# Optimization experiments

Hardware: AMD Instinct MI355X
Metric: run time of the kernel (lower is better)

The kernel has to match this reference:

```python
import jax, jax.numpy as jnp
import numpy as np

B, T, F, C, L, W, NT, H = 4096, 64, 32, 64, 256, 512, 8, 12

# Tsit5 Butcher tableau (fixed-step, 6-stage FSAL-free form)
A21 = 0.161
A31, A32 = -0.008480655492356989, 0.335480655492357
A41, A42, A43 = 2.8971530571054935, -6.359448489975075, 4.362295432869581
A51, A52, A53, A54 = 5.325864828439257, -11.748883564062828, 7.4955393428898365, -0.09249506636175525
A61, A62, A63, A64, A65 = 5.86145544294642, -12.92096931784711, 8.159367898576159, -0.071584973281401, -0.028269050394068383
BC1, BC2, BC3, BC4, BC5, BC6 = 0.09646076681806523, 0.01, 0.4798896504144996, 1.379008574103742, -3.290069515436081, 2.324710524099774
SUBSTEPS = 10  # dt0 = 0.1, integrate each unit interval with 10 fixed steps


def setup_inputs() -> dict:
    key = jax.random.key(0)
    ks = jax.random.split(key, 16)
    def lin(k, out_d, in_d, scale=None):
        s = (1.0 / np.sqrt(in_d)) if scale is None else scale
        return jax.random.normal(k, (out_d, in_d), jnp.float32) * s
    inp = {
        "x_seq": jax.random.normal(ks[0], (B, T, F), jnp.float32),
        "country_idx": jax.random.randint(ks[1], (B,), 0, C),
        "horizon": H,
        # GRU encoder params (equinox GRUCell layout: 3*hidden stacked r,z,n)
        "W_ih": lin(ks[2], 3 * L, F + C),
        "W_hh": lin(ks[3], 3 * L, L),
        "b_ih": jnp.zeros((3 * L,), jnp.float32),
        "b_n": jnp.zeros((L,), jnp.float32),
        # NeuralField MLP 256->512->512->256, small init to keep the ODE stable
        "W0": lin(ks[4], W, L, 0.1 / np.sqrt(L)),
        "b0": jnp.zeros((W,), jnp.float32),
        "W1": lin(ks[5], W, W, 0.1 / np.sqrt(W)),
        "b1": jnp.zeros((W,), jnp.float32),
        "W2": lin(ks[6], L, W, 0.1 / np.sqrt(W)),
        "b2": jnp.zeros((L,), jnp.float32),
        # Decoder
        "W_dec": lin(ks[7], NT, L),
        "b_dec": jnp.zeros((NT,), jnp.float32),
    }
    return inp


def reference(x_seq, W_ih, W_hh, b_ih, b_n, W0, b0, W1, b1, W2, b2, W_dec, b_dec, country_idx, horizon):
    dtype = x_seq.dtype
    n_countries = W_ih.shape[1] - x_seq.shape[2]
    n_latent = W_hh.shape[1]
    ohe = jax.nn.one_hot(country_idx, n_countries, dtype=dtype)  # [B, C]

    # ---- GRU encoder scan over time ----
    h0 = jnp.zeros((x_seq.shape[0], n_latent), dtype)
    def gru_step(h, x_t):
        x_in = jnp.concatenate([x_t, ohe], axis=-1)          # [B, F+C]
        ih = x_in @ W_ih.T + b_ih                            # [B, 3L]
        hh = h @ W_hh.T                                      # [B, 3L]
        ir, iz, inn = jnp.split(ih, 3, axis=-1)
        hr, hz, hn = jnp.split(hh, 3, axis=-1)
        r = jax.nn.sigmoid(ir + hr)
        z = jax.nn.sigmoid(iz + hz)
        n = jnp.tanh(inn + r * (hn + b_n))
        return n + z * (h - n), None
    h_final, _ = jax.lax.scan(gru_step, h0, jnp.swapaxes(x_seq, 0, 1))

    # ---- Neural ODE vector field (autonomous ELU MLP) ----
    def f(y):
        a = jax.nn.elu(y @ W0.T + b0)
        a = jax.nn.elu(a @ W1.T + b1)
        return a @ W2.T + b2

    dt = jnp.asarray(1.0 / SUBSTEPS, dtype)
    def tsit5_step(y, _):
        k1 = f(y)
        k2 = f(y + dt * (A21 * k1))
        k3 = f(y + dt * (A31 * k1 + A32 * k2))
        k4 = f(y + dt * (A41 * k1 + A42 * k2 + A43 * k3))
        k5 = f(y + dt * (A51 * k1 + A52 * k2 + A53 * k3 + A54 * k4))
        k6 = f(y + dt * (A61 * k1 + A62 * k2 + A63 * k3 + A64 * k4 + A65 * k5))
        y_new = y + dt * (BC1 * k1 + BC2 * k2 + BC3 * k3 + BC4 * k4 + BC5 * k5 + BC6 * k6)
        return y_new, None

    def unit(y, _):
        y, _ = jax.lax.scan(tsit5_step, y, None, length=SUBSTEPS)
        return y, y  # save state at each integer time t = 1..horizon

    _, ys = jax.lax.scan(unit, h_final, None, length=horizon)  # [H, B, L]

    # ---- linear decode ----
    out = jnp.einsum('hbl,tl->bht', ys, W_dec) + b_dec  # [B, H, n_targets]
    return out
```

## Files before the change

### kernel.cpp

```cpp
#include <hip/hip_runtime.h>

typedef __bf16 bf16;
typedef __bf16 bf16x8 __attribute__((ext_vector_type(8)));
typedef __bf16 bf16x4 __attribute__((ext_vector_type(4)));
typedef float  f32x4  __attribute__((ext_vector_type(4)));
typedef unsigned int u32;

#define B_TOT 4096
#define T_SEQ 64
#define NT_OUT 8
#define NTHR 512
#define NBLK 256
#define GSZ  8

#define WS_W0   0
#define WS_W1   262144
#define WS_W2   786432
#define WS_WHH  1048576
#define WS_WIH  1441792
#define WS_BC   1490944
#define WS_GY   1703936
#define WS_GYB  3801088
#define WS_GH1  5898240
#define WS_GH2  10092544
#define WS_FLG  14286848
#define WS_MAP  14303232

constexpr float A21 = 0.161f;
constexpr float A31 = -0.008480655492356989f, A32 = 0.335480655492357f;
constexpr float A41 = 2.8971530571054935f, A42 = -6.359448489975075f, A43 = 4.362295432869581f;
constexpr float A51 = 5.325864828439257f, A52 = -11.748883564062828f, A53 = 7.4955393428898365f, A54 = -0.09249506636175525f;
constexpr float A61 = 5.86145544294642f, A62 = -12.92096931784711f, A63 = 8.159367898576159f, A64 = -0.071584973281401f, A65 = -0.028269050394068383f;
constexpr float BC1 = 0.09646076681806523f, BC2 = 0.01f, BC3 = 0.4798896504144996f;
constexpr float BC4 = 1.379008574103742f, BC5 = -3.290069515436081f, BC6 = 2.324710524099774f;
constexpr float DT = 0.1f;
constexpr float BROW[5][5] = {
    {A21, 0, 0, 0, 0},
    {A31, A32, 0, 0, 0},
    {A41, A42, A43, 0, 0},
    {A51, A52, A53, A54, 0},
    {A61, A62, A63, A64, A65}};
constexpr float FCF[6] = {BC1, BC2, BC3, BC4, BC5, BC6};

__device__ __forceinline__ f32x4 MFMA(bf16x8 a, bf16x8 b, f32x4 c) {
    return __builtin_amdgcn_mfma_f32_16x16x32_bf16(a, b, c, 0, 0, 0);
}
__device__ __forceinline__ float eluf(float x) { return x > 0.f ? x : __expf(x) - 1.f; }
__device__ __forceinline__ float sigm_f(float x) { return 1.f / (1.f + __expf(-x)); }
__device__ __forceinline__ float tanh_f(float x) { return 1.f - 2.f / (__expf(2.f * x) + 1.f); }

template<bool FAST>
__device__ __forceinline__ void ld4g(const bf16* p, bf16x8& a0, bf16x8& a1, bf16x8& a2, bf16x8& a3) {
    if constexpr (FAST) {
        asm volatile(
            "global_load_dwordx4 %0, %4, off sc0\n\t"
            "global_load_dwordx4 %1, %4, off offset:1024 sc0\n\t"
            "global_load_dwordx4 %2, %4, off offset:2048 sc0\n\t"
            "global_load_dwordx4 %3, %4, off offset:3072 sc0"
            : "=&v"(a0), "=&v"(a1), "=&v"(a2), "=&v"(a3) : "v"(p) : "memory");
    } else {
        asm volatile(
            "global_load_dwordx4 %0, %4, off sc0 sc1\n\t"
            "global_load_dwordx4 %1, %4, off offset:1024 sc0 sc1\n\t"
            "global_load_dwordx4 %2, %4, off offset:2048 sc0 sc1\n\t"
            "global_load_dwordx4 %3, %4, off offset:3072 sc0 sc1"
            : "=&v"(a0), "=&v"(a1), "=&v"(a2), "=&v"(a3) : "v"(p) : "memory");
    }
}
template<bool FAST>
__device__ __forceinline__ bf16x8 ld1g(const bf16* p) {
    bf16x8 a;
    if constexpr (FAST)
        asm volatile("global_load_dwordx4 %0, %1, off sc0\n\ts_waitcnt vmcnt(0)"
                     : "=v"(a) : "v"(p) : "memory");
    else
        asm volatile("global_load_dwordx4 %0, %1, off sc0 sc1\n\ts_waitcnt vmcnt(0)"
                     : "=v"(a) : "v"(p) : "memory");
    return a;
}
template<bool FAST>
__device__ __forceinline__ void st4g(bf16* p, bf16x4 v) {
    if constexpr (FAST) *(bf16x4*)p = v;
    else asm volatile("global_store_dwordx2 %0, %1, off sc0 sc1" :: "v"(p), "v"(v) : "memory");
}
template<int N>
__device__ __forceinline__ void vmwaitN() {
    asm volatile("s_waitcnt vmcnt(%0)" :: "n"(N) : "memory");
    __builtin_amdgcn_sched_barrier(0);
}

__device__ __forceinline__ void produce(u32* f, int tid) {
    asm volatile("s_waitcnt vmcnt(0)" ::: "memory");
    __syncthreads();
    if (tid == 0) __hip_atomic_fetch_add(f, 1u, __ATOMIC_RELAXED, __HIP_MEMORY_SCOPE_AGENT);
}
__device__ __forceinline__ void consume(const u32* f, u32 tgt, int tid) {
    if (tid == 0) {
        while (__hip_atomic_load(f, __ATOMIC_RELAXED, __HIP_MEMORY_SCOPE_AGENT) < tgt)
            __builtin_amdgcn_s_sleep(1);
    }
    __syncthreads();
}

template<int ST, bool FAST>
__device__ __forceinline__ void ode_stage(
    const bf16* sW0, const bf16* sW1, const bf16* sW2,
    bf16* gY, bf16* gH1, bf16* gH2,
    u32* fY, u32* fH1, u32* fH2, int tid, int w, int lane,
    const f32x4 (&b0v)[4], const f32x4 (&b1v)[4], const f32x4 (&b2v)[2],
    const int (&dA)[4], const int (&dY)[2],
    f32x4 (&yreg)[2], f32x4 (&kreg)[5][2],
    u32& eY, u32& eH1, u32& eH2) {
    const f32x4 Z = {0.f, 0.f, 0.f, 0.f};
    {
        bf16x8 a[8];
        const bf16* p = gY + w * 4096 + lane * 8;
        ld4g<FAST>(p, a[0], a[1], a[2], a[3]);
        ld4g<FAST>(p + 2048, a[4], a[5], a[6], a[7]);
        f32x4 acc[4] = {Z, Z, Z, Z};
        vmwaitN<4>();
        #pragma unroll
        for (int kk = 0; kk < 4; ++kk)
            #pragma unroll
            for (int nt = 0; nt < 4; ++nt)
                acc[nt] = MFMA(*(const bf16x8*)&sW0[(nt * 8 + kk) * 512 + lane * 8], a[kk], acc[nt]);
        vmwaitN<0>();
        #pragma unroll
        for (int kk = 4; kk < 8; ++kk)
            #pragma unroll
            for (int nt = 0; nt < 4; ++nt)
                acc[nt] = MFMA(*(const bf16x8*)&sW0[(nt * 8 + kk) * 512 + lane * 8], a[kk], acc[nt]);
        #pragma unroll
        for (int nt = 0; nt < 4; ++nt) {
            bf16x4 ov;
            #pragma unroll
            for (int r = 0; r < 4; ++r) ov[r] = (bf16)eluf(acc[nt][r] + b0v[nt][r]);
            st4g<FAST>(gH1 + w * 8192 + dA[nt], ov);
        }
    }
    produce(fH1, tid); ++eH1;
    consume(fH1, GSZ * eH1, tid);
    {
        bf16x8 a[16];
        const bf16* p = gH1 + w * 8192 + lane * 8;
        ld4g<FAST>(p, a[0], a[1], a[2], a[3]);
        ld4g<FAST>(p + 2048, a[4], a[5], a[6], a[7]);
        ld4g<FAST>(p + 4096, a[8], a[9], a[10], a[11]);
        ld4g<FAST>(p + 6144, a[12], a[13], a[14], a[15]);
        f32x4 acc[4] = {Z, Z, Z, Z};
        vmwaitN<8>();
        #pragma unroll
        for (int kk = 0; kk < 8; ++kk)
            #pragma unroll
            for (int nt = 0; nt < 4; ++nt)
                acc[nt] = MFMA(*(const bf16x8*)&sW1[(nt * 16 + kk) * 512 + lane * 8], a[kk], acc[nt]);
        vmwaitN<0>();
        #pragma unroll
        for (int kk = 8; kk < 16; ++kk)
            #pragma unroll
            for (int nt = 0; nt < 4; ++nt)
                acc[nt] = MFMA(*(const bf16x8*)&sW1[(nt * 16 + kk) * 512 + lane * 8], a[kk], acc[nt]);
        #pragma unroll
        for (int nt = 0; nt < 4; ++nt) {
            bf16x4 ov;
            #pragma unroll
            for (int r = 0; r < 4; ++r) ov[r] = (bf16)eluf(acc[nt][r] + b1v[nt][r]);
            st4g<FAST>(gH2 + w * 8192 + dA[nt], ov);
        }
    }
    produce(fH2, tid); ++eH2;
    consume(fH2, GSZ * eH2, tid);
    {
        bf16x8 a[16];
        const bf16* p = gH2 + w * 8192 + lane * 8;
        ld4g<FAST>(p, a[0], a[1], a[2], a[3]);
        ld4g<FAST>(p + 2048, a[4], a[5], a[6], a[7]);
        ld4g<FAST>(p + 4096, a[8], a[9], a[10], a[11]);
        ld4g<FAST>(p + 6144, a[12], a[13], a[14], a[15]);
        f32x4 acc[2] = {Z, Z};
        vmwaitN<8>();
        #pragma unroll
        for (int kk = 0; kk < 8; ++kk)
            #pragma unroll
            for (int nt = 0; nt < 2; ++nt)
                acc[nt] = MFMA(*(const bf16x8*)&sW2[(nt * 16 + kk) * 512 + lane * 8], a[kk], acc[nt]);
        vmwaitN<0>();
        #pragma unroll
        for (int kk = 8; kk < 16; ++kk)
            #pragma unroll
            for (int nt = 0; nt < 2; ++nt)
                acc[nt] = MFMA(*(const bf16x8*)&sW2[(nt * 16 + kk) * 512 + lane * 8], a[kk], acc[nt]);
        #pragma unroll
        for (int nt = 0; nt < 2; ++nt) {
            f32x4 kv;
            #pragma unroll
            for (int r = 0; r < 4; ++r) kv[r] = acc[nt][r] + b2v[nt][r];
            f32x4 yst;
            if constexpr (ST < 5) {
                kreg[ST][nt] = kv;
                yst = yreg[nt];
                #pragma unroll
                for (int s = 0; s <= ST; ++s) {
                    const float c = DT * BROW[ST][s];
                    #pragma unroll
                    for (int r = 0; r < 4; ++r) yst[r] += c * kreg[s][nt][r];
                }
            } else {
                #pragma unroll
                for (int s = 0; s < 5; ++s) {
                    const float c = DT * FCF[s];
                    #pragma unroll
                    for (int r = 0; r < 4; ++r) yreg[nt][r] += c * kreg[s][nt][r];
                }
                #pragma unroll
                for (int r = 0; r < 4; ++r) yreg[nt][r] += (DT * FCF[5]) * kv[r];
                yst = yreg[nt];
            }
            bf16x4 ov;
            #pragma unroll
            for (int r = 0; r < 4; ++r) ov[r] = (bf16)yst[r];
            st4g<FAST>(gY + w * 4096 + dY[nt], ov);
        }
    }
    produce(fY, tid); ++eY;
}

template<bool FAST>
__device__ __forceinline__ void dec_unit(const bf16* gY, const float* sWdec, const float* sBdec,
                                         float* out, int g, int j, int w, int lane, int H, int u) {
    const int rloc = 2 * w + (lane >> 5);
    const int li = lane & 31;
    const bf16* p = gY + (size_t)j * 4096 + (((li >> 2) * 64 + (li & 3) * 16 + rloc)) * 8;
    bf16x8 yv = ld1g<FAST>(p);
    const int f0 = li * 8;
    float acc[8];
    #pragma unroll
    for (int t = 0; t < 8; ++t) acc[t] = 0.f;
    #pragma unroll
    for (int e = 0; e < 8; ++e) {
        const float yf = (float)yv[e];
        #pragma unroll
        for (int t = 0; t < 8; ++t) acc[t] += yf * sWdec[t * 256 + f0 + e];
    }
    #pragma unroll
    for (int k = 1; k < 32; k <<= 1)
        #pragma unroll
        for (int t = 0; t < 8; ++t) acc[t] += __shfl_xor(acc[t], k, 64);
    if (li == 0) {
        const size_t row = (size_t)g * 128 + 16 * j + rloc;
        #pragma unroll
        for (int t = 0; t < 8; ++t) out[(row * H + u) * NT_OUT + t] = acc[t] + sBdec[t];
    }
}

template<bool FAST>
__device__ void body(const float* __restrict__ x_seq, const int* __restrict__ cidx,
                     const float* __restrict__ b_n, const float* __restrict__ b0,
                     const float* __restrict__ b1, const float* __restrict__ b2,
                     const float* __restrict__ W_dec, const float* __restrict__ b_dec,
                     char* __restrict__ ws, float* __restrict__ out,
                     bf16* sWgt, float* sWdec, float* sBdec,
                     int H, int g, int j) {
    const int tid = threadIdx.x, w = tid >> 6, lane = tid & 63;
    const int lm = lane & 15, q = lane >> 4, q4 = q << 2;
    const int grow0 = g * 128;

    const bf16* W0p  = (const bf16*)(ws + WS_W0);
    const bf16* W1p  = (const bf16*)(ws + WS_W1);
    const bf16* W2p  = (const bf16*)(ws + WS_W2);
    const bf16* WhhP = (const bf16*)(ws + WS_WHH);
    const bf16* WihP = (const bf16*)(ws + WS_WIH);
    const float* bias_c = (const float*)(ws + WS_BC);
    bf16* gY  = (bf16*)(ws + WS_GY)  + (size_t)g * 32768;
    bf16* gYb = (bf16*)(ws + WS_GYB) + (size_t)g * 32768;
    bf16* gH1 = (bf16*)(ws + WS_GH1) + (size_t)g * 65536;
    bf16* gH2 = (bf16*)(ws + WS_GH2) + (size_t)g * 65536;
    u32* fl  = (u32*)(ws + WS_FLG + (size_t)g * 512);
    u32 *fY = fl, *fH1 = fl + 16, *fH2 = fl + 32;

    u32 eY = 0, eH1 = 0, eH2 = 0;

    for (int i = tid; i < 2048; i += NTHR) sWdec[i] = W_dec[i];
    if (tid < 8) sBdec[tid] = b_dec[tid];
    for (int i = tid; i < 54 * 64; i += NTHR) {
        const int fr = i >> 6, l = i & 63;
        const int tau = fr / 9, kk = fr % 9;
        const int gam = tau >> 1, p = tau & 1;
        const int c = gam * 16 + 2 * j + p;
        const bf16* src = (kk < 8) ? &WhhP[(((size_t)c) * 8 + kk) * 512 + l * 8]
                                   : &WihP[((size_t)c) * 512 + l * 8];
        *(bf16x8*)&sWgt[((size_t)fr) * 512 + l * 8] = *(const bf16x8*)src;
    }

    const int m = w;
    float bcr[2][4], bcz[2][4], bcn[2][4], bnr[2][4];
    {
        const int c = cidx[grow0 + 16 * m + lm];
        #pragma unroll
        for (int p = 0; p < 2; ++p)
            #pragma unroll
            for (int r = 0; r < 4; ++r) {
                const int F = 32 * j + p * 16 + q4 + r;
                bcr[p][r] = bias_c[(size_t)c * 768 + F];
                bcz[p][r] = bias_c[(size_t)c * 768 + 256 + F];
                bcn[p][r] = bias_c[(size_t)c * 768 + 512 + F];
                bnr[p][r] = b_n[F];
            }
    }
    int dY[2];
    #pragma unroll
    for (int p = 0; p < 2; ++p)
        dY[p] = (j * 64 + ((4 * j + 2 * p + (q >> 1)) & 3) * 16 + lm) * 8 + (q & 1) * 4;

    {
        bf16x4 z4;
        #pragma unroll
        for (int r = 0; r < 4; ++r) z4[r] = (bf16)0.f;
        st4g<FAST>(gY + m * 4096 + dY[0], z4);
        st4g<FAST>(gY + m * 4096 + dY[1], z4);
    }
    produce(fY, tid); ++eY;

    f32x4 hreg[2] = {{0.f, 0.f, 0.f, 0.f}, {0.f, 0.f, 0.f, 0.f}};
    const f32x4 Z = {0.f, 0.f, 0.f, 0.f};
    for (int t = 0; t < T_SEQ; ++t) {
        bf16x8 ax;
        {
            const float* xp = x_seq + (((size_t)(grow0 + 16 * m + lm)) * T_SEQ + t) * 32 + q * 8;
            f32x4 xa = *(const f32x4*)xp;
            f32x4 xb = *(const f32x4*)(xp + 4);
            #pragma unroll
            for (int e = 0; e < 4; ++e) { ax[e] = (bf16)xa[e]; ax[4 + e] = (bf16)xb[e]; }
        }
        consume(fY, GSZ * eY, tid);
        const bf16* hs = ((t & 1) ? gYb : gY) + m * 4096 + lane * 8;
        bf16x8 a[8];
        ld4g<FAST>(hs, a[0], a[1], a[2], a[3]);
        ld4g<FAST>(hs + 2048, a[4], a[5], a[6], a[7]);
        f32x4 rz[4] = {Z, Z, Z, Z}, nH[2] = {Z, Z}, nX[2] = {Z, Z};
        vmwaitN<4>();
        #pragma unroll
        for (int kk = 0; kk < 4; ++kk) {
            #pragma unroll
            for (int p = 0; p < 2; ++p) {
                rz[p]     = MFMA(*(const bf16x8*)&sWgt[((0 + p) * 9 + kk) * 512 + lane * 8], a[kk], rz[p]);
                rz[2 + p] = MFMA(*(const bf16x8*)&sWgt[((2 + p) * 9 + kk) * 512 + lane * 8], a[kk], rz[2 + p]);
                nH[p]     = MFMA(*(const bf16x8*)&sWgt[((4 + p) * 9 + kk) * 512 + lane * 8], a[kk], nH[p]);
            }
        }
        vmwaitN<0>();
        #pragma unroll
        for (int kk = 4; kk < 8; ++kk) {
            #pragma unroll
            for (int p = 0; p < 2; ++p) {
                rz[p]     = MFMA(*(const bf16x8*)&sWgt[((0 + p) * 9 + kk) * 512 + lane * 8], a[kk], rz[p]);
                rz[2 + p] = MFMA(*(const bf16x8*)&sWgt[((2 + p) * 9 + kk) * 512 + lane * 8], a[kk], rz[2 + p]);
                nH[p]     = MFMA(*(const bf16x8*)&sWgt[((4 + p) * 9 + kk) * 512 + lane * 8], a[kk], nH[p]);
            }
        }
        #pragma unroll
        for (int p = 0; p < 2; ++p) {
            rz[p]     = MFMA(*(const bf16x8*)&sWgt[((0 + p) * 9 + 8) * 512 + lane * 8], ax, rz[p]);
            rz[2 + p] = MFMA(*(const bf16x8*)&sWgt[((2 + p) * 9 + 8) * 512 + lane * 8], ax, rz[2 + p]);
            nX[p]     = MFMA(*(const bf16x8*)&sWgt[((4 + p) * 9 + 8) * 512 + lane * 8], ax, nX[p]);
        }
        bf16* hd = (((t + 1) & 1) ? gYb : gY) + m * 4096;
        #pragma unroll
        for (int p = 0; p < 2; ++p) {
            bf16x4 ov;
            #pragma unroll
            for (int r = 0; r < 4; ++r) {
                const float rg = sigm_f(rz[p][r] + bcr[p][r]);
                const float zg = sigm_f(rz[2 + p][r] + bcz[p][r]);
                const float nn = tanh_f(nX[p][r] + bcn[p][r] + rg * (nH[p][r] + bnr[p][r]));
                hreg[p][r] = nn + zg * (hreg[p][r] - nn);
                ov[r] = (bf16)hreg[p][r];
            }
            st4g<FAST>(hd + dY[p], ov);
        }
        produce(fY, tid); ++eY;
    }

    bf16* sW0 = sWgt;
    bf16* sW1 = sWgt + 16384;
    bf16* sW2 = sWgt + 49152;
    for (int i = tid; i < 2048; i += NTHR)
        *(bf16x8*)&sW0[i * 8] = *(const bf16x8*)&W0p[(size_t)j * 16384 + i * 8];
    for (int i = tid; i < 4096; i += NTHR)
        *(bf16x8*)&sW1[i * 8] = *(const bf16x8*)&W1p[(size_t)j * 32768 + i * 8];
    for (int i = tid; i < 2048; i += NTHR)
        *(bf16x8*)&sW2[i * 8] = *(const bf16x8*)&W2p[(size_t)j * 16384 + i * 8];
    __syncthreads();

    f32x4 b0v[4], b1v[4], b2v[2];
    #pragma unroll
    for (int nt = 0; nt < 4; ++nt) {
        b0v[nt] = *(const f32x4*)&b0[64 * j + nt * 16 + q4];
        b1v[nt] = *(const f32x4*)&b1[64 * j + nt * 16 + q4];
    }
    #pragma unroll
    for (int nt = 0; nt < 2; ++nt) b2v[nt] = *(const f32x4*)&b2[32 * j + nt * 16 + q4];
    int dA[4];
    #pragma unroll
    for (int nt = 0; nt < 4; ++nt)
        dA[nt] = ((2 * j + (nt >> 1)) * 64 + ((8 * j + 2 * nt + (q >> 1)) & 3) * 16 + lm) * 8 + (q & 1) * 4;

    f32x4 yreg[2] = {hreg[0], hreg[1]};
    f32x4 kreg[5][2];

    const int NSS = H * 10;
    for (int ss = 0; ss < NSS; ++ss) {
        consume(fY, GSZ * eY, tid);
        if (ss && ss % 10 == 0)
            dec_unit<FAST>(gY, sWdec, sBdec, out, g, j, w, lane, H, ss / 10 - 1);
        ode_stage<0, FAST>(sW0, sW1, sW2, gY, gH1, gH2, fY, fH1, fH2, tid, w, lane,
                           b0v, b1v, b2v, dA, dY, yreg, kreg, eY, eH1, eH2);
        consume(fY, GSZ * eY, tid);
        ode_stage<1, FAST>(sW0, sW1, sW2, gY, gH1, gH2, fY, fH1, fH2, tid, w, lane,
                           b0v, b1v, b2v, dA, dY, yreg, kreg, eY, eH1, eH2);
        consume(fY, GSZ * eY, tid);
        ode_stage<2, FAST>(sW0, sW1, sW2, gY, gH1, gH2, fY, fH1, fH2, tid, w, lane,
                           b0v, b1v, b2v, dA, dY, yreg, kreg, eY, eH1, eH2);
        consume(fY, GSZ * eY, tid);
        ode_stage<3, FAST>(sW0, sW1, sW2, gY, gH1, gH2, fY, fH1, fH2, tid, w, lane,
                           b0v, b1v, b2v, dA, dY, yreg, kreg, eY, eH1, eH2);
        consume(fY, GSZ * eY, tid);
        ode_stage<4, FAST>(sW0, sW1, sW2, gY, gH1, gH2, fY, fH1, fH2, tid, w, lane,
                           b0v, b1v, b2v, dA, dY, yreg, kreg, eY, eH1, eH2);
        consume(fY, GSZ * eY, tid);
        ode_stage<5, FAST>(sW0, sW1, sW2, gY, gH1, gH2, fY, fH1, fH2, tid, w, lane,
                           b0v, b1v, b2v, dA, dY, yreg, kreg, eY, eH1, eH2);
    }
    consume(fY, GSZ * eY, tid);
    dec_unit<FAST>(gY, sWdec, sBdec, out, g, j, w, lane, H, H - 1);
}

__global__ void __launch_bounds__(NTHR, 2)
k_main(const float* __restrict__ x_seq, const int* __restrict__ cidx,
       const float* __restrict__ b_n, const float* __restrict__ b0,
       const float* __restrict__ b1, const float* __restrict__ b2,
       const float* __restrict__ W_dec, const float* __restrict__ b_dec,
       char* __restrict__ ws, float* __restrict__ out, int H) {
    __shared__ __align__(16) bf16 sWgt[65536];
    __shared__ __align__(16) float sWdec[2048];
    __shared__ float sBdec[8];
    __shared__ u32 mapL[NBLK];
    __shared__ int sMeta[3];

    const int tid = threadIdx.x, b = blockIdx.x;

    u32* xmap = (u32*)(ws + WS_MAP);
    u32* gctr = (u32*)(ws + WS_MAP + 1024);
    u32 xcc;
    asm volatile("s_getreg_b32 %0, hwreg(HW_REG_XCC_ID)" : "=s"(xcc));
    if (tid == 0) {
        __hip_atomic_store(&xmap[b], xcc, __ATOMIC_RELEASE, __HIP_MEMORY_SCOPE_AGENT);
        __hip_atomic_fetch_add(gctr, 1u, __ATOMIC_ACQ_REL, __HIP_MEMORY_SCOPE_AGENT);
        while (__hip_atomic_load(gctr, __ATOMIC_ACQUIRE, __HIP_MEMORY_SCOPE_AGENT) < NBLK)
            __builtin_amdgcn_s_sleep(8);
    }
    __syncthreads();
    if (tid < NBLK)
        mapL[tid] = __hip_atomic_load(&xmap[tid], __ATOMIC_ACQUIRE, __HIP_MEMORY_SCOPE_AGENT);
    __syncthreads();

    if (tid == 0) {
        int cnt[8] = {0, 0, 0, 0, 0, 0, 0, 0};
        int rank = 0, bad = 0;
        const u32 my = mapL[b];
        for (int i = 0; i < NBLK; ++i) {
            const u32 x = mapL[i];
            if (x > 7u) bad = 1;
            else cnt[x]++;
            if (i < b && x == my) ++rank;
        }
        int ok = !bad;
        #pragma unroll
        for (int i = 0; i < 8; ++i) ok &= (cnt[i] == 32);
        sMeta[0] = ok;
        sMeta[1] = ok ? (int)(my * 4 + (rank >> 3)) : ((b & 7) * 4 + (b >> 6));
        sMeta[2] = ok ? (rank & 7) : ((b >> 3) & 7);
    }
    __syncthreads();
    const int ok = sMeta[0], g = sMeta[1], j = sMeta[2];
    __syncthreads();

    if (ok)
        body<true>(x_seq, cidx, b_n, b0, b1, b2, W_dec, b_dec, ws, out,
                   sWgt, sWdec, sBdec, H, g, j);
    else
        body<false>(x_seq, cidx, b_n, b0, b1, b2, W_dec, b_dec, ws, out,
                    sWgt, sWdec, sBdec, H, g, j);
}

__global__ void k_pack(const float* __restrict__ src, bf16* __restrict__ dst,
                       int OUT, int K, int Ksrc, int koff) {
    const int total = (OUT * K) >> 3;
    for (int gg = blockIdx.x * blockDim.x + threadIdx.x; gg < total; gg += gridDim.x * blockDim.x) {
        const int lane = gg & 63, f = gg >> 6;
        const int KK = K >> 5;
        const int kk = f % KK, c = f / KK;
        const int col = c * 16 + (lane & 15);
        const int k0 = kk * 32 + ((lane >> 4) << 3);
        bf16x8 o;
        #pragma unroll
        for (int jj = 0; jj < 8; ++jj) o[jj] = (bf16)src[(size_t)col * Ksrc + koff + k0 + jj];
        *(bf16x8*)&dst[(size_t)gg * 8] = o;
    }
}

__global__ void k_bias(const float* __restrict__ W_ih, const float* __restrict__ b_ih,
                       float* __restrict__ bias_c) {
    const int i = blockIdx.x * blockDim.x + threadIdx.x;
    if (i < 64 * 768) {
        const int c = i / 768, n = i - c * 768;
        bias_c[i] = W_ih[(size_t)n * 96 + 32 + c] + b_ih[n];
    }
}

extern "C" void kernel_launch(void* const* d_in, const int* in_sizes, int n_in,
                              void* d_out, int out_size, void* d_ws, size_t ws_size,
                              hipStream_t stream) {
    const float* x_seq = (const float*)d_in[0];
    const int*   cidx  = (const int*)d_in[1];
    const float* W_ih  = (const float*)d_in[3];
    const float* W_hh  = (const float*)d_in[4];
    const float* b_ih  = (const float*)d_in[5];
    const float* b_n   = (const float*)d_in[6];
    const float* W0    = (const float*)d_in[7];
    const float* b0    = (const float*)d_in[8];
    const float* W1    = (const float*)d_in[9];
    const float* b1    = (const float*)d_in[10];
    const float* W2    = (const float*)d_in[11];
    const float* b2    = (const float*)d_in[12];
    const float* W_dec = (const float*)d_in[13];
    const float* b_dec = (const float*)d_in[14];
    float* out = (float*)d_out;
    const int H = out_size / (B_TOT * NT_OUT);
    char* ws = (char*)d_ws;

    hipMemsetAsync(ws + WS_FLG, 0, 20480, stream);

    k_pack<<<64, 256, 0, stream>>>(W0, (bf16*)(ws + WS_W0), 512, 256, 256, 0);
    k_pack<<<128, 256, 0, stream>>>(W1, (bf16*)(ws + WS_W1), 512, 512, 512, 0);
    k_pack<<<64, 256, 0, stream>>>(W2, (bf16*)(ws + WS_W2), 256, 512, 512, 0);
    k_pack<<<96, 256, 0, stream>>>(W_hh, (bf16*)(ws + WS_WHH), 768, 256, 256, 0);
    k_pack<<<12, 256, 0, stream>>>(W_ih, (bf16*)(ws + WS_WIH), 768, 32, 96, 0);
    k_bias<<<(64 * 768 + 255) / 256, 256, 0, stream>>>(W_ih, b_ih, (float*)(ws + WS_BC));

    k_main<<<NBLK, NTHR, 0, stream>>>(x_seq, cidx, b_n, b0, b1, b2, W_dec, b_dec,
                                      ws, out, H);
}
```

Before: 5.656 ms.

## Fold W0 into W2 and carry ODE state in first-layer preactivation space

The ODE state is now tracked as u = W0·y + b0 (512-wide pre-activation) instead of y. The second layer's output is multiplied by a precomputed fused matrix W0·W2 to update u directly, so the per-stage W0 GEMM and one cross-block y synchronization per stage disappear. y itself is still accumulated via W2 (read from global memory) and only published at unit boundaries for decoding. The cost is a larger fused GEMM (512 wide instead of 256), extra per-block scratch for stage products stored in bf16, and extra global W2 reads. Numerics also change because the fused weights are rounded to bf16.

```diff
diff --git a/kernel.cpp b/kernel.cpp
--- a/kernel.cpp
+++ b/kernel.cpp
@@ -19,12 +19,15 @@
 #define WS_WHH  1048576
 #define WS_WIH  1441792
 #define WS_BC   1490944
-#define WS_GY   1703936
-#define WS_GYB  3801088
-#define WS_GH1  5898240
-#define WS_GH2  10092544
-#define WS_FLG  14286848
-#define WS_MAP  14303232
+#define WS_PB   1687552
+#define WS_WFP  1689600
+#define WS_GY   2213888
+#define WS_GYB  4311040
+#define WS_GH1  6408192
+#define WS_GH2  10602496
+#define WS_GP   14796800
+#define WS_FLG  35768320
+#define WS_MAP  35784704
 
 constexpr float A21 = 0.161f;
 constexpr float A31 = -0.008480655492356989f, A32 = 0.335480655492357f;
@@ -104,42 +107,35 @@
 
 template<int ST, bool FAST>
 __device__ __forceinline__ void ode_stage(
-    const bf16* sW0, const bf16* sW1, const bf16* sW2,
-    bf16* gY, bf16* gH1, bf16* gH2,
-    u32* fY, u32* fH1, u32* fH2, int tid, int w, int lane,
-    const f32x4 (&b0v)[4], const f32x4 (&b1v)[4], const f32x4 (&b2v)[2],
+    const bf16* sW1, const bf16* sWF, const bf16* __restrict__ W2j,
+    bf16* gY, bf16* gH1, bf16* gH2, bf16* __restrict__ gPblk,
+    u32* fH1, u32* fH2, int tid, int w, int lane,
+    const f32x4 (&b1v)[4], const f32x4 (&b2v)[2], const f32x4 (&pbv)[4],
     const int (&dA)[4], const int (&dY)[2],
-    f32x4 (&yreg)[2], f32x4 (&kreg)[5][2],
-    u32& eY, u32& eH1, u32& eH2) {
+    f32x4 (&u)[4], f32x4 (&du)[4], f32x4 (&yv)[2],
+    u32& eH1, u32& eH2, bool bnd) {
     const f32x4 Z = {0.f, 0.f, 0.f, 0.f};
-    {
-        bf16x8 a[8];
-        const bf16* p = gY + w * 4096 + lane * 8;
-        ld4g<FAST>(p, a[0], a[1], a[2], a[3]);
-        ld4g<FAST>(p + 2048, a[4], a[5], a[6], a[7]);
-        f32x4 acc[4] = {Z, Z, Z, Z};
-        vmwaitN<4>();
-        #pragma unroll
-        for (int kk = 0; kk < 4; ++kk)
-            #pragma unroll
-            for (int nt = 0; nt < 4; ++nt)
-                acc[nt] = MFMA(*(const bf16x8*)&sW0[(nt * 8 + kk) * 512 + lane * 8], a[kk], acc[nt]);
-        vmwaitN<0>();
-        #pragma unroll
-        for (int kk = 4; kk < 8; ++kk)
-            #pragma unroll
-            for (int nt = 0; nt < 4; ++nt)
-                acc[nt] = MFMA(*(const bf16x8*)&sW0[(nt * 8 + kk) * 512 + lane * 8], a[kk], acc[nt]);
-        #pragma unroll
-        for (int nt = 0; nt < 4; ++nt) {
-            bf16x4 ov;
-            #pragma unroll
-            for (int r = 0; r < 4; ++r) ov[r] = (bf16)eluf(acc[nt][r] + b0v[nt][r]);
-            st4g<FAST>(gH1 + w * 8192 + dA[nt], ov);
-        }
+
+    #pragma unroll
+    for (int nt = 0; nt < 4; ++nt) {
+        f32x4 v = u[nt];
+        if constexpr (ST > 0) {
+            #pragma unroll
+            for (int l = 0; l < ST; ++l) {
+                bf16x4 pv = *(const bf16x4*)&gPblk[l * 8192 + ((w * 4 + nt) * 64 + lane) * 4];
+                const float c = DT * BROW[ST - 1][l];
+                #pragma unroll
+                for (int r = 0; r < 4; ++r) v[r] += c * (float)pv[r];
+            }
+        }
+        bf16x4 ov;
+        #pragma unroll
+        for (int r = 0; r < 4; ++r) ov[r] = (bf16)eluf(v[r]);
+        st4g<FAST>(gH1 + w * 8192 + dA[nt], ov);
     }
     produce(fH1, tid); ++eH1;
     consume(fH1, GSZ * eH1, tid);
+
     {
         bf16x8 a[16];
         const bf16* p = gH1 + w * 8192 + lane * 8;
@@ -170,6 +166,7 @@
     }
     produce(fH2, tid); ++eH2;
     consume(fH2, GSZ * eH2, tid);
+
     {
         bf16x8 a[16];
         const bf16* p = gH2 + w * 8192 + lane * 8;
@@ -177,57 +174,65 @@
         ld4g<FAST>(p + 2048, a[4], a[5], a[6], a[7]);
         ld4g<FAST>(p + 4096, a[8], a[9], a[10], a[11]);
         ld4g<FAST>(p + 6144, a[12], a[13], a[14], a[15]);
-        f32x4 acc[2] = {Z, Z};
+        f32x4 accp[4] = {Z, Z, Z, Z};
         vmwaitN<8>();
         #pragma unroll
         for (int kk = 0; kk < 8; ++kk)
             #pragma unroll
+            for (int nt = 0; nt < 4; ++nt)
+                accp[nt] = MFMA(*(const bf16x8*)&sWF[(nt * 16 + kk) * 512 + lane * 8], a[kk], accp[nt]);
+        vmwaitN<0>();
+        #pragma unroll
+        for (int kk = 8; kk < 16; ++kk)
+            #pragma unroll
+            for (int nt = 0; nt < 4; ++nt)
+                accp[nt] = MFMA(*(const bf16x8*)&sWF[(nt * 16 + kk) * 512 + lane * 8], a[kk], accp[nt]);
+        #pragma unroll
+        for (int nt = 0; nt < 4; ++nt) {
+            f32x4 pp;
+            #pragma unroll
+            for (int r = 0; r < 4; ++r) pp[r] = accp[nt][r] + pbv[nt][r];
+            #pragma unroll
+            for (int r = 0; r < 4; ++r) du[nt][r] += (DT * FCF[ST]) * pp[r];
+            if constexpr (ST < 5) {
+                bf16x4 o;
+                #pragma unroll
+                for (int r = 0; r < 4; ++r) o[r] = (bf16)pp[r];
+                *(bf16x4*)&gPblk[ST * 8192 + ((w * 4 + nt) * 64 + lane) * 4] = o;
+            }
+        }
+        if constexpr (ST == 5) {
+            #pragma unroll
+            for (int nt = 0; nt < 4; ++nt)
+                #pragma unroll
+                for (int r = 0; r < 4; ++r) u[nt][r] += du[nt][r];
+        }
+        f32x4 acck[2] = {Z, Z};
+        #pragma unroll
+        for (int kk = 0; kk < 16; ++kk)
+            #pragma unroll
             for (int nt = 0; nt < 2; ++nt)
-                acc[nt] = MFMA(*(const bf16x8*)&sW2[(nt * 16 + kk) * 512 + lane * 8], a[kk], acc[nt]);
-        vmwaitN<0>();
-        #pragma unroll
-        for (int kk = 8; kk < 16; ++kk)
-            #pragma unroll
-            for (int nt = 0; nt < 2; ++nt)
-                acc[nt] = MFMA(*(const bf16x8*)&sW2[(nt * 16 + kk) * 512 + lane * 8], a[kk], acc[nt]);
-        #pragma unroll
-        for (int nt = 0; nt < 2; ++nt) {
-            f32x4 kv;
-            #pragma unroll
-            for (int r = 0; r < 4; ++r) kv[r] = acc[nt][r] + b2v[nt][r];
-            f32x4 yst;
-            if constexpr (ST < 5) {
-                kreg[ST][nt] = kv;
-                yst = yreg[nt];
+                acck[nt] = MFMA(*(const bf16x8*)&W2j[(nt * 16 + kk) * 512 + lane * 8], a[kk], acck[nt]);
+        #pragma unroll
+        for (int nt = 0; nt < 2; ++nt)
+            #pragma unroll
+            for (int r = 0; r < 4; ++r)
+                yv[nt][r] += (DT * FCF[ST]) * (acck[nt][r] + b2v[nt][r]);
+        if (bnd) {
+            #pragma unroll
+            for (int nt = 0; nt < 2; ++nt) {
+                bf16x4 o;
                 #pragma unroll
-                for (int s = 0; s <= ST; ++s) {
-                    const float c = DT * BROW[ST][s];
-                    #pragma unroll
-                    for (int r = 0; r < 4; ++r) yst[r] += c * kreg[s][nt][r];
-                }
-            } else {
-                #pragma unroll
-                for (int s = 0; s < 5; ++s) {
-                    const float c = DT * FCF[s];
-                    #pragma unroll
-                    for (int r = 0; r < 4; ++r) yreg[nt][r] += c * kreg[s][nt][r];
-                }
-                #pragma unroll
-                for (int r = 0; r < 4; ++r) yreg[nt][r] += (DT * FCF[5]) * kv[r];
-                yst = yreg[nt];
+                for (int r = 0; r < 4; ++r) o[r] = (bf16)yv[nt][r];
+                st4g<FAST>(gY + w * 4096 + dY[nt], o);
             }
-            bf16x4 ov;
-            #pragma unroll
-            for (int r = 0; r < 4; ++r) ov[r] = (bf16)yst[r];
-            st4g<FAST>(gY + w * 4096 + dY[nt], ov);
-        }
-    }
-    produce(fY, tid); ++eY;
+        }
+    }
 }
 
 template<bool FAST>
 __device__ __forceinline__ void dec_unit(const bf16* gY, const float* sWdec, const float* sBdec,
-                                         float* out, int g, int j, int w, int lane, int H, int u) {
+                                         float* out, int g, int j, int w, int lane, int H, int uu) {
     const int rloc = 2 * w + (lane >> 5);
     const int li = lane & 31;
     const bf16* p = gY + (size_t)j * 4096 + (((li >> 2) * 64 + (li & 3) * 16 + rloc)) * 8;
@@ -249,7 +254,7 @@
     if (li == 0) {
         const size_t row = (size_t)g * 128 + 16 * j + rloc;
         #pragma unroll
-        for (int t = 0; t < 8; ++t) out[(row * H + u) * NT_OUT + t] = acc[t] + sBdec[t];
+        for (int t = 0; t < 8; ++t) out[(row * H + uu) * NT_OUT + t] = acc[t] + sBdec[t];
     }
 }
 
@@ -260,7 +265,7 @@
                      const float* __restrict__ W_dec, const float* __restrict__ b_dec,
                      char* __restrict__ ws, float* __restrict__ out,
                      bf16* sWgt, float* sWdec, float* sBdec,
-                     int H, int g, int j) {
+                     int H, int g, int j, int bglob) {
     const int tid = threadIdx.x, w = tid >> 6, lane = tid & 63;
     const int lm = lane & 15, q = lane >> 4, q4 = q << 2;
     const int grow0 = g * 128;
@@ -270,11 +275,14 @@
     const bf16* W2p  = (const bf16*)(ws + WS_W2);
     const bf16* WhhP = (const bf16*)(ws + WS_WHH);
     const bf16* WihP = (const bf16*)(ws + WS_WIH);
+    const bf16* WFp  = (const bf16*)(ws + WS_WFP);
     const float* bias_c = (const float*)(ws + WS_BC);
+    const float* pb  = (const float*)(ws + WS_PB);
     bf16* gY  = (bf16*)(ws + WS_GY)  + (size_t)g * 32768;
     bf16* gYb = (bf16*)(ws + WS_GYB) + (size_t)g * 32768;
     bf16* gH1 = (bf16*)(ws + WS_GH1) + (size_t)g * 65536;
     bf16* gH2 = (bf16*)(ws + WS_GH2) + (size_t)g * 65536;
+    bf16* gPblk = (bf16*)(ws + WS_GP) + (size_t)bglob * 40960;
     u32* fl  = (u32*)(ws + WS_FLG + (size_t)g * 512);
     u32 *fY = fl, *fH1 = fl + 16, *fH2 = fl + 32;
 
@@ -381,22 +389,47 @@
         produce(fY, tid); ++eY;
     }
 
-    bf16* sW0 = sWgt;
-    bf16* sW1 = sWgt + 16384;
-    bf16* sW2 = sWgt + 49152;
+    consume(fY, GSZ * eY, tid);
+
     for (int i = tid; i < 2048; i += NTHR)
-        *(bf16x8*)&sW0[i * 8] = *(const bf16x8*)&W0p[(size_t)j * 16384 + i * 8];
+        *(bf16x8*)&sWgt[i * 8] = *(const bf16x8*)&W0p[(size_t)j * 16384 + i * 8];
+    __syncthreads();
+    f32x4 u[4], du[4], yv[2];
+    {
+        bf16x8 a[8];
+        const bf16* p = gY + w * 4096 + lane * 8;
+        ld4g<FAST>(p, a[0], a[1], a[2], a[3]);
+        ld4g<FAST>(p + 2048, a[4], a[5], a[6], a[7]);
+        f32x4 acc[4] = {Z, Z, Z, Z};
+        vmwaitN<0>();
+        #pragma unroll
+        for (int kk = 0; kk < 8; ++kk)
+            #pragma unroll
+            for (int nt = 0; nt < 4; ++nt)
+                acc[nt] = MFMA(*(const bf16x8*)&sWgt[(nt * 8 + kk) * 512 + lane * 8], a[kk], acc[nt]);
+        #pragma unroll
+        for (int nt = 0; nt < 4; ++nt) {
+            f32x4 b0v = *(const f32x4*)&b0[64 * j + nt * 16 + q4];
+            #pragma unroll
+            for (int r = 0; r < 4; ++r) u[nt][r] = acc[nt][r] + b0v[r];
+        }
+    }
+    __syncthreads();
+
     for (int i = tid; i < 4096; i += NTHR)
-        *(bf16x8*)&sW1[i * 8] = *(const bf16x8*)&W1p[(size_t)j * 32768 + i * 8];
-    for (int i = tid; i < 2048; i += NTHR)
-        *(bf16x8*)&sW2[i * 8] = *(const bf16x8*)&W2p[(size_t)j * 16384 + i * 8];
-    __syncthreads();
-
-    f32x4 b0v[4], b1v[4], b2v[2];
+        *(bf16x8*)&sWgt[i * 8] = *(const bf16x8*)&W1p[(size_t)j * 32768 + i * 8];
+    for (int i = tid; i < 4096; i += NTHR)
+        *(bf16x8*)&sWgt[32768 + i * 8] = *(const bf16x8*)&WFp[(size_t)j * 32768 + i * 8];
+    __syncthreads();
+    const bf16* sW1 = sWgt;
+    const bf16* sWF = sWgt + 32768;
+    const bf16* W2j = W2p + (size_t)j * 16384;
+
+    f32x4 b1v[4], pbv[4], b2v[2];
     #pragma unroll
     for (int nt = 0; nt < 4; ++nt) {
-        b0v[nt] = *(const f32x4*)&b0[64 * j + nt * 16 + q4];
         b1v[nt] = *(const f32x4*)&b1[64 * j + nt * 16 + q4];
+        pbv[nt] = *(const f32x4*)&pb[64 * j + nt * 16 + q4];
     }
     #pragma unroll
     for (int nt = 0; nt < 2; ++nt) b2v[nt] = *(const f32x4*)&b2[32 * j + nt * 16 + q4];
@@ -404,35 +437,31 @@
     #pragma unroll
     for (int nt = 0; nt < 4; ++nt)
         dA[nt] = ((2 * j + (nt >> 1)) * 64 + ((8 * j + 2 * nt + (q >> 1)) & 3) * 16 + lm) * 8 + (q & 1) * 4;
-
-    f32x4 yreg[2] = {hreg[0], hreg[1]};
-    f32x4 kreg[5][2];
+    yv[0] = hreg[0]; yv[1] = hreg[1];
 
     const int NSS = H * 10;
     for (int ss = 0; ss < NSS; ++ss) {
-        consume(fY, GSZ * eY, tid);
-        if (ss && ss % 10 == 0)
-            dec_unit<FAST>(gY, sWdec, sBdec, out, g, j, w, lane, H, ss / 10 - 1);
-        ode_stage<0, FAST>(sW0, sW1, sW2, gY, gH1, gH2, fY, fH1, fH2, tid, w, lane,
-                           b0v, b1v, b2v, dA, dY, yreg, kreg, eY, eH1, eH2);
-        consume(fY, GSZ * eY, tid);
-        ode_stage<1, FAST>(sW0, sW1, sW2, gY, gH1, gH2, fY, fH1, fH2, tid, w, lane,
-                           b0v, b1v, b2v, dA, dY, yreg, kreg, eY, eH1, eH2);
-        consume(fY, GSZ * eY, tid);
-        ode_stage<2, FAST>(sW0, sW1, sW2, gY, gH1, gH2, fY, fH1, fH2, tid, w, lane,
-                           b0v, b1v, b2v, dA, dY, yreg, kreg, eY, eH1, eH2);
-        consume(fY, GSZ * eY, tid);
-        ode_stage<3, FAST>(sW0, sW1, sW2, gY, gH1, gH2, fY, fH1, fH2, tid, w, lane,
-                           b0v, b1v, b2v, dA, dY, yreg, kreg, eY, eH1, eH2);
-        consume(fY, GSZ * eY, tid);
-        ode_stage<4, FAST>(sW0, sW1, sW2, gY, gH1, gH2, fY, fH1, fH2, tid, w, lane,
-                           b0v, b1v, b2v, dA, dY, yreg, kreg, eY, eH1, eH2);
-        consume(fY, GSZ * eY, tid);
-        ode_stage<5, FAST>(sW0, sW1, sW2, gY, gH1, gH2, fY, fH1, fH2, tid, w, lane,
-                           b0v, b1v, b2v, dA, dY, yreg, kreg, eY, eH1, eH2);
-    }
-    consume(fY, GSZ * eY, tid);
-    dec_unit<FAST>(gY, sWdec, sBdec, out, g, j, w, lane, H, H - 1);
+        const bool bnd = ((ss % 10) == 9);
+        #pragma unroll
+        for (int nt = 0; nt < 4; ++nt) du[nt] = Z;
+        ode_stage<0, FAST>(sW1, sWF, W2j, gY, gH1, gH2, gPblk, fH1, fH2, tid, w, lane,
+                           b1v, b2v, pbv, dA, dY, u, du, yv, eH1, eH2, false);
+        ode_stage<1, FAST>(sW1, sWF, W2j, gY, gH1, gH2, gPblk, fH1, fH2, tid, w, lane,
+                           b1v, b2v, pbv, dA, dY, u, du, yv, eH1, eH2, false);
+        ode_stage<2, FAST>(sW1, sWF, W2j, gY, gH1, gH2, gPblk, fH1, fH2, tid, w, lane,
+                           b1v, b2v, pbv, dA, dY, u, du, yv, eH1, eH2, false);
+        ode_stage<3, FAST>(sW1, sWF, W2j, gY, gH1, gH2, gPblk, fH1, fH2, tid, w, lane,
+                           b1v, b2v, pbv, dA, dY, u, du, yv, eH1, eH2, false);
+        ode_stage<4, FAST>(sW1, sWF, W2j, gY, gH1, gH2, gPblk, fH1, fH2, tid, w, lane,
+                           b1v, b2v, pbv, dA, dY, u, du, yv, eH1, eH2, false);
+        ode_stage<5, FAST>(sW1, sWF, W2j, gY, gH1, gH2, gPblk, fH1, fH2, tid, w, lane,
+                           b1v, b2v, pbv, dA, dY, u, du, yv, eH1, eH2, bnd);
+        if (bnd) {
+            produce(fY, tid); ++eY;
+            consume(fY, GSZ * eY, tid);
+            dec_unit<FAST>(gY, sWdec, sBdec, out, g, j, w, lane, H, ss / 10);
+        }
+    }
 }
 
 __global__ void __launch_bounds__(NTHR, 2)
@@ -487,10 +516,10 @@
 
     if (ok)
         body<true>(x_seq, cidx, b_n, b0, b1, b2, W_dec, b_dec, ws, out,
-                   sWgt, sWdec, sBdec, H, g, j);
+                   sWgt, sWdec, sBdec, H, g, j, b);
     else
         body<false>(x_seq, cidx, b_n, b0, b1, b2, W_dec, b_dec, ws, out,
-                    sWgt, sWdec, sBdec, H, g, j);
+                    sWgt, sWdec, sBdec, H, g, j, b);
 }
 
 __global__ void k_pack(const float* __restrict__ src, bf16* __restrict__ dst,
@@ -506,6 +535,27 @@
         #pragma unroll
         for (int jj = 0; jj < 8; ++jj) o[jj] = (bf16)src[(size_t)col * Ksrc + koff + k0 + jj];
         *(bf16x8*)&dst[(size_t)gg * 8] = o;
+    }
+}
+
+__global__ void k_fuse(const float* __restrict__ W0, const float* __restrict__ W2,
+                       bf16* __restrict__ WFp) {
+    const int o = blockIdx.x;
+    const int i = threadIdx.x;
+    float s = 0.f;
+    for (int mm = 0; mm < 256; ++mm) s += W0[(size_t)o * 256 + mm] * W2[(size_t)mm * 512 + i];
+    const int c = o >> 4, lanelo = o & 15, kk = i >> 5, within = i & 31;
+    const int lane = lanelo | ((within >> 3) << 4), jj = within & 7;
+    WFp[((size_t)(c * 16 + kk)) * 512 + lane * 8 + jj] = (bf16)s;
+}
+
+__global__ void k_pb(const float* __restrict__ W0, const float* __restrict__ b2,
+                     float* __restrict__ pb) {
+    const int o = blockIdx.x * blockDim.x + threadIdx.x;
+    if (o < 512) {
+        float s = 0.f;
+        for (int mm = 0; mm < 256; ++mm) s += b2[mm] * W0[(size_t)o * 256 + mm];
+        pb[o] = s;
     }
 }
 
@@ -547,6 +597,8 @@
     k_pack<<<96, 256, 0, stream>>>(W_hh, (bf16*)(ws + WS_WHH), 768, 256, 256, 0);
     k_pack<<<12, 256, 0, stream>>>(W_ih, (bf16*)(ws + WS_WIH), 768, 32, 96, 0);
     k_bias<<<(64 * 768 + 255) / 256, 256, 0, stream>>>(W_ih, b_ih, (float*)(ws + WS_BC));
+    k_fuse<<<512, 512, 0, stream>>>(W0, W2, (bf16*)(ws + WS_WFP));
+    k_pb<<<2, 256, 0, stream>>>(W0, b2, (float*)(ws + WS_PB));
 
     k_main<<<NBLK, NTHR, 0, stream>>>(x_seq, cidx, b_n, b0, b1, b2, W_dec, b_dec,
                                       ws, out, H);
```

Result: slower. 15.44 ms (+173.1%).
